# Kernel tuning notes

Hardware: AMD Instinct MI355X
Metric: run time of the kernel (lower is better)

The kernel has to match this reference:

```python
import jax, jax.numpy as jnp
import numpy as np

N, E, EL, D_IN, D_H = 100000, 1600000, 200000, 128, 128

def setup_inputs() -> dict:
    key = jax.random.key(0)
    ks = jax.random.split(key, 12)
    glorot = lambda k, fi, fo: jax.random.normal(k, (fi, fo), jnp.float32) * np.sqrt(2.0 / (fi + fo))
    return {
        "x": jax.random.normal(ks[0], (N, D_IN), jnp.float32),
        "edge_index": jax.random.randint(ks[1], (2, E), 0, N, jnp.int64),
        "edge_label_index": jax.random.randint(ks[2], (2, EL), 0, N, jnp.int64),
        "W1": glorot(ks[3], D_IN, D_H), "b1": jnp.zeros((D_H,), jnp.float32),
        "W2": glorot(ks[4], D_H, D_H), "b2": jnp.zeros((D_H,), jnp.float32),
        "Wp1": glorot(ks[5], 2 * D_H, D_H), "bp1": jnp.zeros((D_H,), jnp.float32),
        "Wp2": glorot(ks[6], D_H, 1), "bp2": jnp.zeros((1,), jnp.float32),
    }

def gcn_conv(x, W, b, src, dst, n_nodes):
    # GCNConv: h = D^{-1/2} (A + I) D^{-1/2} (x @ W) + b, deg includes self-loop
    h = x @ W                                            # [N, D]
    deg = jnp.zeros((n_nodes,), h.dtype).at[dst].add(1.0) + 1.0
    dinv = jax.lax.rsqrt(deg)                            # [N]
    coef = dinv[src] * dinv[dst]                         # [E]
    agg = jnp.zeros_like(h).at[dst].add(h[src] * coef[:, None])
    agg = agg + h * (dinv * dinv)[:, None]               # self-loop term
    return agg + b

def reference(x, edge_index, edge_label_index, W1, b1, W2, b2, Wp1, bp1, Wp2, bp2):
    src, dst = edge_index[0], edge_index[1]
    n = x.shape[0]
    h = jax.nn.relu(gcn_conv(x, W1, b1, src, dst, n))
    h = gcn_conv(h, W2, b2, src, dst, n)
    # link scoring: gather src/dst embeddings, concat, 2-layer MLP (dropout = eval identity)
    edge_emb = jnp.concatenate([h[edge_label_index[0]], h[edge_label_index[1]]], axis=1)  # [EL, 2D]
    pred = jax.nn.relu(edge_emb @ Wp1 + bp1) @ Wp2 + bp2
    return pred.squeeze(-1)
```

## Files before the change

kernel.cpp:

```cpp
#include <hip/hip_runtime.h>

#define NN 100000
#define EE 1600000
#define ELN 200000

#define NB 98
#define BKT_SHIFT 10
#define BKT_NODES 1024
#define MSB 256
#define EPB (EE / MSB)

typedef __attribute__((ext_vector_type(4))) float f32x4;
typedef __attribute__((ext_vector_type(8))) short short8;

__device__ __forceinline__ unsigned short f2bf(float f) {
    unsigned u = __builtin_bit_cast(unsigned, f);
    u += 0x7FFF + ((u >> 16) & 1);
    return (unsigned short)(u >> 16);
}
__device__ __forceinline__ float bf2f(unsigned short h) {
    return __builtin_bit_cast(float, (unsigned)h << 16);
}

__device__ __forceinline__ void convw_one(const float* __restrict__ W,
                                          unsigned short* __restrict__ WT, int K, int u) {
    int n = u & 127, kq = u >> 7;
    short8 t;
#pragma unroll
    for (int j = 0; j < 8; j++)
        t[j] = (short)f2bf(W[(size_t)(kq * 8 + j) * 128 + n]);
    *(short8*)(WT + (size_t)n * K + kq * 8) = t;
}

__global__ __launch_bounds__(256) void convw_kernel(const float* __restrict__ W1,
                                                    const float* __restrict__ W2,
                                                    const float* __restrict__ Wp1,
                                                    unsigned short* __restrict__ W1T,
                                                    unsigned short* __restrict__ W2T,
                                                    unsigned short* __restrict__ WpT) {
    int u = blockIdx.x * 256 + threadIdx.x;
    if (u < 2048) convw_one(W1, W1T, 128, u);
    else if (u < 4096) convw_one(W2, W2T, 128, u - 2048);
    else convw_one(Wp1, WpT, 256, u - 4096);
}

__global__ __launch_bounds__(256) void ms_hist_kernel(const int* __restrict__ dst,
                                                      int* __restrict__ histM) {
    __shared__ int cnt[NB];
    int tid = threadIdx.x;
    if (tid < NB) cnt[tid] = 0;
    __syncthreads();
    int base = blockIdx.x * EPB;
    for (int i = tid; i < EPB; i += 256)
        atomicAdd(&cnt[dst[base + i] >> BKT_SHIFT], 1);
    __syncthreads();
    if (tid < NB) histM[tid * MSB + blockIdx.x] = cnt[tid];
}

__global__ __launch_bounds__(256) void ms_scan_kernel(int* __restrict__ histM,
                                                      int* __restrict__ rowptr) {
    __shared__ int sm[256];
    int tid = threadIdx.x;
    const int CPT = NB * MSB / 256;
    int base = tid * CPT;
    int s = 0;
    for (int i = 0; i < CPT; i++) s += histM[base + i];
    sm[tid] = s;
    __syncthreads();
    for (int off = 1; off < 256; off <<= 1) {
        int add = (tid >= off) ? sm[tid - off] : 0;
        __syncthreads();
        sm[tid] += add;
        __syncthreads();
    }
    int run = sm[tid] - s;
    for (int i = 0; i < CPT; i++) {
        int v = histM[base + i];
        histM[base + i] = run;
        run += v;
    }
    if (tid == 0) rowptr[NN] = EE;
}

__global__ __launch_bounds__(256) void ms_scatter_kernel(const int* __restrict__ src,
                                                         const int* __restrict__ dst,
                                                         const int* __restrict__ histO,
                                                         unsigned* __restrict__ tmp) {
    __shared__ int off[NB];
    int tid = threadIdx.x;
    if (tid < NB) off[tid] = histO[tid * MSB + blockIdx.x];
    __syncthreads();
    int base = blockIdx.x * EPB;
    for (int i = tid; i < EPB; i += 256) {
        int d = dst[base + i];
        int s = src[base + i];
        int b = d >> BKT_SHIFT;
        int pos = atomicAdd(&off[b], 1);
        tmp[pos] = ((unsigned)(d & (BKT_NODES - 1)) << 17) | (unsigned)s;
    }
}

__global__ __launch_bounds__(256) void bucket_csr_kernel(const unsigned* __restrict__ tmp,
                                                         const int* __restrict__ histO,
                                                         int* __restrict__ rowptr,
                                                         float* __restrict__ dinv,
                                                         int* __restrict__ csr) {
    __shared__ int cnt[BKT_NODES];
    __shared__ int lp[BKT_NODES];
    __shared__ int sm[256];
    int b = blockIdx.x;
    int tid = threadIdx.x;
    int gbase = histO[b * MSB];
    int gend = (b == NB - 1) ? EE : histO[(b + 1) * MSB];
    for (int i = tid; i < BKT_NODES; i += 256) cnt[i] = 0;
    __syncthreads();
    for (int i = gbase + tid; i < gend; i += 256)
        atomicAdd(&cnt[tmp[i] >> 17], 1);
    __syncthreads();
    int s0 = cnt[tid * 4], s1 = cnt[tid * 4 + 1], s2 = cnt[tid * 4 + 2], s3 = cnt[tid * 4 + 3];
    int tot = s0 + s1 + s2 + s3;
    sm[tid] = tot;
    __syncthreads();
    for (int off = 1; off < 256; off <<= 1) {
        int add = (tid >= off) ? sm[tid - off] : 0;
        __syncthreads();
        sm[tid] += add;
        __syncthreads();
    }
    int excl = sm[tid] - tot;
    lp[tid * 4] = excl;
    lp[tid * 4 + 1] = excl + s0;
    lp[tid * 4 + 2] = excl + s0 + s1;
    lp[tid * 4 + 3] = excl + s0 + s1 + s2;
    int n0 = b << BKT_SHIFT;
#pragma unroll
    for (int q = 0; q < 4; q++) {
        int i = tid * 4 + q;
        int node = n0 + i;
        if (node < NN) {
            rowptr[node] = gbase + (q == 0 ? excl : lp[i]);
            int c = (q == 0) ? s0 : (q == 1 ? s1 : (q == 2 ? s2 : s3));
            dinv[node] = rsqrtf((float)c + 1.0f);
        }
    }
    cnt[tid * 4] = 0; cnt[tid * 4 + 1] = 0; cnt[tid * 4 + 2] = 0; cnt[tid * 4 + 3] = 0;
    __syncthreads();
    for (int i = gbase + tid; i < gend; i += 256) {
        unsigned p = tmp[i];
        int dl = p >> 17;
        int s = p & 0x1FFFF;
        int pos = atomicAdd(&cnt[dl], 1);
        csr[gbase + lp[dl] + pos] = s;
    }
}

template <int AMODE>
__global__ __launch_bounds__(256) void gemm_mfma_kernel(const void* __restrict__ Av,
                                                        const unsigned short* __restrict__ WT,
                                                        const float* __restrict__ dinv,
                                                        unsigned short* __restrict__ out,
                                                        int nchunks) {
    __shared__ __align__(16) char Wl[128 * 128 * 2];
    int tid = threadIdx.x;
#pragma unroll
    for (int j = 0; j < 8; j++) {
        int slot = tid + j * 256;
        int n = slot >> 4, k0 = (slot & 15) * 8;
        int byte = (n * 256 + k0 * 2) ^ ((n & 7) << 4);
        *(short8*)(Wl + byte) = ((const short8*)WT)[slot];
    }
    __syncthreads();
    int wid = tid >> 6, l = tid & 63;
    int lhi = l >> 4, llo = l & 15;
    for (int chunk = blockIdx.x; chunk < nchunks; chunk += gridDim.x) {
        int r0 = chunk * 64 + wid * 16;
        int arow = r0 + llo;
        f32x4 acc[8];
#pragma unroll
        for (int c = 0; c < 8; c++) acc[c] = (f32x4)0.0f;
#pragma unroll
        for (int ks = 0; ks < 4; ks++) {
            int koff = ks * 32 + lhi * 8;
            short8 a;
            if (arow < NN) {
                if (AMODE == 0) {
                    const float* ap = (const float*)Av + (size_t)arow * 128 + koff;
                    float4 v0 = *(const float4*)ap;
                    float4 v1 = *(const float4*)(ap + 4);
                    a[0] = (short)f2bf(v0.x); a[1] = (short)f2bf(v0.y);
                    a[2] = (short)f2bf(v0.z); a[3] = (short)f2bf(v0.w);
                    a[4] = (short)f2bf(v1.x); a[5] = (short)f2bf(v1.y);
                    a[6] = (short)f2bf(v1.z); a[7] = (short)f2bf(v1.w);
                } else {
                    a = *(const short8*)((const unsigned short*)Av + (size_t)arow * 128 + koff);
                }
            } else {
                a = (short8)(short)0;
            }
#pragma unroll
            for (int c = 0; c < 8; c++) {
                int n = c * 16 + llo;
                int byte = (n * 256 + koff * 2) ^ ((n & 7) << 4);
                short8 bfr = *(const short8*)(Wl + byte);
                acc[c] = __builtin_amdgcn_mfma_f32_16x16x32_bf16(a, bfr, acc[c], 0, 0, 0);
            }
        }
        float dv[4];
#pragma unroll
        for (int j = 0; j < 4; j++) {
            int row = r0 + lhi * 4 + j;
            dv[j] = (row < NN) ? dinv[row] : 0.f;
        }
#pragma unroll
        for (int c = 0; c < 8; c++) {
            int col = c * 16 + llo;
#pragma unroll
            for (int j = 0; j < 4; j++) {
                int row = r0 + lhi * 4 + j;
                if (row < NN)
                    out[(size_t)row * 128 + col] = f2bf(acc[c][j] * dv[j]);
            }
        }
    }
}

template <int RELU>
__global__ __launch_bounds__(256) void agg_row_kernel(const unsigned short* __restrict__ g,
                                                      const int* __restrict__ rowptr,
                                                      const int* __restrict__ csr,
                                                      const float* __restrict__ dinv,
                                                      const float* __restrict__ bias,
                                                      unsigned short* __restrict__ out) {
    int wid = threadIdx.x >> 6, l = threadIdx.x & 63;
    int node = blockIdx.x * 4 + wid;
    if (node >= NN) return;
    const unsigned* gp = (const unsigned*)g;
    unsigned sv = gp[(size_t)node * 64 + l];
    float a0 = bf2f((unsigned short)sv);
    float a1 = bf2f((unsigned short)(sv >> 16));
    int beg = rowptr[node], end = rowptr[node + 1];
    int i = beg;
    for (; i + 8 <= end; i += 8) {
        int s[8];
        unsigned v[8];
#pragma unroll
        for (int j = 0; j < 8; j++) s[j] = csr[i + j];
#pragma unroll
        for (int j = 0; j < 8; j++) v[j] = gp[(size_t)s[j] * 64 + l];
#pragma unroll
        for (int j = 0; j < 8; j++) {
            a0 += bf2f((unsigned short)v[j]);
            a1 += bf2f((unsigned short)(v[j] >> 16));
        }
    }
    for (; i < end; i++) {
        int s = csr[i];
        unsigned v = gp[(size_t)s * 64 + l];
        a0 += bf2f((unsigned short)v);
        a1 += bf2f((unsigned short)(v >> 16));
    }
    float dn = dinv[node];
    a0 = fmaf(dn, a0, bias[l * 2]);
    a1 = fmaf(dn, a1, bias[l * 2 + 1]);
    if (RELU) { a0 = fmaxf(a0, 0.f); a1 = fmaxf(a1, 0.f); }
    ((unsigned*)out)[(size_t)node * 64 + l] = (unsigned)f2bf(a0) | ((unsigned)f2bf(a1) << 16);
}

__global__ __launch_bounds__(512, 2) void link_mfma_kernel(const unsigned short* __restrict__ h,
                                                           const int* __restrict__ eli,
                                                           const unsigned short* __restrict__ WpT,
                                                           const float* __restrict__ bp1,
                                                           const float* __restrict__ Wp2,
                                                           const float* __restrict__ bp2,
                                                           float* __restrict__ out) {
    __shared__ __align__(16) char Wl[128 * 256 * 2];
    int tid = threadIdx.x;
#pragma unroll
    for (int j = 0; j < 8; j++) {
        int slot = tid + j * 512;
        int n = slot >> 5, k0 = (slot & 31) * 8;
        int byte = (n * 512 + k0 * 2) ^ ((n & 7) << 4);
        *(short8*)(Wl + byte) = ((const short8*)WpT)[slot];
    }
    __syncthreads();
    int wid = tid >> 6, l = tid & 63;
    int lhi = l >> 4, llo = l & 15;
    float b2 = bp2[0];
    const int NG = (ELN + 127) / 128;
    for (int g = blockIdx.x; g < NG; g += gridDim.x) {
        int e_base = g * 128 + wid * 16;
        if (e_base >= ELN) continue;
        int ea = e_base + llo;
        int es = eli[ea], et = eli[ELN + ea];
        f32x4 acc[8];
#pragma unroll
        for (int c = 0; c < 8; c++) acc[c] = (f32x4)0.0f;
#pragma unroll
        for (int ks = 0; ks < 8; ks++) {
            int kg = ks * 32 + lhi * 8;
            int row = (kg < 128) ? es : et;
            int koff = kg & 127;
            short8 a = *(const short8*)(h + (size_t)row * 128 + koff);
#pragma unroll
            for (int c = 0; c < 8; c++) {
                int n = c * 16 + llo;
                int byte = (n * 512 + kg * 2) ^ ((n & 7) << 4);
                short8 bfr = *(const short8*)(Wl + byte);
                acc[c] = __builtin_amdgcn_mfma_f32_16x16x32_bf16(a, bfr, acc[c], 0, 0, 0);
            }
        }
        float p0 = 0.f, p1 = 0.f, p2 = 0.f, p3 = 0.f;
#pragma unroll
        for (int c = 0; c < 8; c++) {
            int col = c * 16 + llo;
            float bb = bp1[col];
            float w2 = Wp2[col];
            p0 += fmaxf(acc[c][0] + bb, 0.f) * w2;
            p1 += fmaxf(acc[c][1] + bb, 0.f) * w2;
            p2 += fmaxf(acc[c][2] + bb, 0.f) * w2;
            p3 += fmaxf(acc[c][3] + bb, 0.f) * w2;
        }
#pragma unroll
        for (int off = 1; off < 16; off <<= 1) {
            p0 += __shfl_xor(p0, off);
            p1 += __shfl_xor(p1, off);
            p2 += __shfl_xor(p2, off);
            p3 += __shfl_xor(p3, off);
        }
        if (llo == 0) {
            int e = e_base + lhi * 4;
            out[e + 0] = p0 + b2;
            out[e + 1] = p1 + b2;
            out[e + 2] = p2 + b2;
            out[e + 3] = p3 + b2;
        }
    }
}

extern "C" void kernel_launch(void* const* d_in, const int* in_sizes, int n_in,
                              void* d_out, int out_size, void* d_ws, size_t ws_size,
                              hipStream_t stream) {
    const float* x   = (const float*)d_in[0];
    const int*   ei  = (const int*)d_in[1];
    const int*   eli = (const int*)d_in[2];
    const float* W1  = (const float*)d_in[3];
    const float* b1  = (const float*)d_in[4];
    const float* W2  = (const float*)d_in[5];
    const float* b2  = (const float*)d_in[6];
    const float* Wp1 = (const float*)d_in[7];
    const float* bp1 = (const float*)d_in[8];
    const float* Wp2 = (const float*)d_in[9];
    const float* bp2 = (const float*)d_in[10];
    float* out = (float*)d_out;

    char* w = (char*)d_ws;
    auto alloc = [&](size_t bytes) {
        char* p = w;
        w += (bytes + 255) & ~(size_t)255;
        return p;
    };
    float*          dinv   = (float*)alloc((size_t)NN * 4);
    int*            rowptr = (int*)alloc((size_t)(NN + 1) * 4);
    int*            histM  = (int*)alloc((size_t)NB * MSB * 4);
    unsigned*       tmp    = (unsigned*)alloc((size_t)EE * 4);
    int*            csr    = (int*)alloc((size_t)EE * 4);
    unsigned short* gbuf   = (unsigned short*)alloc((size_t)NN * 128 * 2);
    unsigned short* hbuf   = (unsigned short*)alloc((size_t)NN * 128 * 2);
    unsigned short* W1T    = (unsigned short*)alloc((size_t)128 * 128 * 2);
    unsigned short* W2T    = (unsigned short*)alloc((size_t)128 * 128 * 2);
    unsigned short* WpT    = (unsigned short*)alloc((size_t)128 * 256 * 2);

    const int* srcv = ei;
    const int* dstv = ei + EE;

    convw_kernel<<<32, 256, 0, stream>>>(W1, W2, Wp1, W1T, W2T, WpT);

    ms_hist_kernel<<<MSB, 256, 0, stream>>>(dstv, histM);
    ms_scan_kernel<<<1, 256, 0, stream>>>(histM, rowptr);
    ms_scatter_kernel<<<MSB, 256, 0, stream>>>(srcv, dstv, histM, tmp);
    bucket_csr_kernel<<<NB, 256, 0, stream>>>(tmp, histM, rowptr, dinv, csr);

    int nchunks = (NN + 63) / 64;
    gemm_mfma_kernel<0><<<1024, 256, 0, stream>>>(x, W1T, dinv, gbuf, nchunks);
    agg_row_kernel<1><<<NN / 4, 256, 0, stream>>>(gbuf, rowptr, csr, dinv, b1, hbuf);
    gemm_mfma_kernel<1><<<1024, 256, 0, stream>>>(hbuf, W2T, dinv, gbuf, nchunks);
    agg_row_kernel<0><<<NN / 4, 256, 0, stream>>>(gbuf, rowptr, csr, dinv, b2, hbuf);
    link_mfma_kernel<<<512, 512, 0, stream>>>(hbuf, eli, WpT, bp1, Wp2, bp2, out);
}
```

Baseline: 310.1 us.

## Fuse layer-1 aggregation with layer-2 GEMM and widen aggregation to 16-byte gathers

Layer-1 aggregation now runs inside a new kernel: each wave aggregates 16 node rows into LDS, then multiplies them by W2 with MFMA and writes the dinv-scaled g2 directly. This removes one kernel launch and the round trip of the hidden activations through global memory. The aggregation kernels also switch from one lane per 2 features to 16 lanes per node, each doing short8 (16-byte) loads, so four nodes are handled per wave. The cost is a larger LDS footprint per block, which may reduce occupancy, and a serial aggregate-then-GEMM phase inside each wave.

```diff
diff --git a/kernel.cpp b/kernel.cpp
--- a/kernel.cpp
+++ b/kernel.cpp
@@ -154,8 +154,7 @@
     }
 }
 
-template <int AMODE>
-__global__ __launch_bounds__(256) void gemm_mfma_kernel(const void* __restrict__ Av,
+__global__ __launch_bounds__(256) void gemm_mfma_kernel(const float* __restrict__ Av,
                                                         const unsigned short* __restrict__ WT,
                                                         const float* __restrict__ dinv,
                                                         unsigned short* __restrict__ out,
@@ -183,17 +182,13 @@
             int koff = ks * 32 + lhi * 8;
             short8 a;
             if (arow < NN) {
-                if (AMODE == 0) {
-                    const float* ap = (const float*)Av + (size_t)arow * 128 + koff;
-                    float4 v0 = *(const float4*)ap;
-                    float4 v1 = *(const float4*)(ap + 4);
-                    a[0] = (short)f2bf(v0.x); a[1] = (short)f2bf(v0.y);
-                    a[2] = (short)f2bf(v0.z); a[3] = (short)f2bf(v0.w);
-                    a[4] = (short)f2bf(v1.x); a[5] = (short)f2bf(v1.y);
-                    a[6] = (short)f2bf(v1.z); a[7] = (short)f2bf(v1.w);
-                } else {
-                    a = *(const short8*)((const unsigned short*)Av + (size_t)arow * 128 + koff);
-                }
+                const float* ap = Av + (size_t)arow * 128 + koff;
+                float4 v0 = *(const float4*)ap;
+                float4 v1 = *(const float4*)(ap + 4);
+                a[0] = (short)f2bf(v0.x); a[1] = (short)f2bf(v0.y);
+                a[2] = (short)f2bf(v0.z); a[3] = (short)f2bf(v0.w);
+                a[4] = (short)f2bf(v1.x); a[5] = (short)f2bf(v1.y);
+                a[6] = (short)f2bf(v1.z); a[7] = (short)f2bf(v1.w);
             } else {
                 a = (short8)(short)0;
             }
@@ -224,46 +219,150 @@
     }
 }
 
-template <int RELU>
-__global__ __launch_bounds__(256) void agg_row_kernel(const unsigned short* __restrict__ g,
-                                                      const int* __restrict__ rowptr,
-                                                      const int* __restrict__ csr,
-                                                      const float* __restrict__ dinv,
-                                                      const float* __restrict__ bias,
-                                                      unsigned short* __restrict__ out) {
-    int wid = threadIdx.x >> 6, l = threadIdx.x & 63;
-    int node = blockIdx.x * 4 + wid;
+__global__ __launch_bounds__(512) void agg1_gemm2_kernel(const unsigned short* __restrict__ g1,
+                                                         const unsigned short* __restrict__ W2T,
+                                                         const int* __restrict__ rowptr,
+                                                         const int* __restrict__ csr,
+                                                         const float* __restrict__ dinv,
+                                                         const float* __restrict__ b1,
+                                                         unsigned short* __restrict__ g2) {
+    __shared__ __align__(16) char Wl[128 * 128 * 2];
+    __shared__ __align__(16) char Ht[8][16 * 128 * 2];
+    int tid = threadIdx.x;
+#pragma unroll
+    for (int j = 0; j < 4; j++) {
+        int slot = tid + j * 512;
+        int n = slot >> 4, k0 = (slot & 15) * 8;
+        int byte = (n * 256 + k0 * 2) ^ ((n & 7) << 4);
+        *(short8*)(Wl + byte) = ((const short8*)W2T)[slot];
+    }
+    __syncthreads();
+    int w = tid >> 6, l = tid & 63;
+    int t = l >> 4, q = l & 15;
+    char* ht = Ht[w];
+    int base = blockIdx.x * 128 + w * 16;
+    float bb[8];
+#pragma unroll
+    for (int j = 0; j < 8; j++) bb[j] = b1[q * 8 + j];
+#pragma unroll
+    for (int tb = 0; tb < 4; tb++) {
+        int node = base + tb * 4 + t;
+        float a[8];
+#pragma unroll
+        for (int j = 0; j < 8; j++) a[j] = 0.f;
+        if (node < NN) {
+            short8 sv = *(const short8*)(g1 + (size_t)node * 128 + q * 8);
+#pragma unroll
+            for (int j = 0; j < 8; j++) a[j] += bf2f((unsigned short)sv[j]);
+            int beg = rowptr[node], end = rowptr[node + 1];
+            int i = beg;
+            for (; i + 4 <= end; i += 4) {
+                int s0 = csr[i], s1 = csr[i + 1], s2 = csr[i + 2], s3 = csr[i + 3];
+                short8 v0 = *(const short8*)(g1 + (size_t)s0 * 128 + q * 8);
+                short8 v1 = *(const short8*)(g1 + (size_t)s1 * 128 + q * 8);
+                short8 v2 = *(const short8*)(g1 + (size_t)s2 * 128 + q * 8);
+                short8 v3 = *(const short8*)(g1 + (size_t)s3 * 128 + q * 8);
+#pragma unroll
+                for (int j = 0; j < 8; j++) {
+                    a[j] += bf2f((unsigned short)v0[j]);
+                    a[j] += bf2f((unsigned short)v1[j]);
+                    a[j] += bf2f((unsigned short)v2[j]);
+                    a[j] += bf2f((unsigned short)v3[j]);
+                }
+            }
+            for (; i < end; i++) {
+                int s = csr[i];
+                short8 v = *(const short8*)(g1 + (size_t)s * 128 + q * 8);
+#pragma unroll
+                for (int j = 0; j < 8; j++) a[j] += bf2f((unsigned short)v[j]);
+            }
+            float dn = dinv[node];
+#pragma unroll
+            for (int j = 0; j < 8; j++) a[j] = fmaxf(fmaf(dn, a[j], bb[j]), 0.f);
+        }
+        short8 hr;
+#pragma unroll
+        for (int j = 0; j < 8; j++) hr[j] = (short)f2bf(a[j]);
+        int r = tb * 4 + t;
+        int byte = (r * 256 + q * 16) ^ ((r & 7) << 4);
+        *(short8*)(ht + byte) = hr;
+    }
+    int llo = q, lhi = t;
+    f32x4 acc[8];
+#pragma unroll
+    for (int c = 0; c < 8; c++) acc[c] = (f32x4)0.0f;
+#pragma unroll
+    for (int ks = 0; ks < 4; ks++) {
+        int koff = ks * 32 + lhi * 8;
+        int abyte = (llo * 256 + koff * 2) ^ ((llo & 7) << 4);
+        short8 afr = *(const short8*)(ht + abyte);
+#pragma unroll
+        for (int c = 0; c < 8; c++) {
+            int n = c * 16 + llo;
+            int byte = (n * 256 + koff * 2) ^ ((n & 7) << 4);
+            short8 bfr = *(const short8*)(Wl + byte);
+            acc[c] = __builtin_amdgcn_mfma_f32_16x16x32_bf16(afr, bfr, acc[c], 0, 0, 0);
+        }
+    }
+    float dv[4];
+#pragma unroll
+    for (int j = 0; j < 4; j++) {
+        int row = base + lhi * 4 + j;
+        dv[j] = (row < NN) ? dinv[row] : 0.f;
+    }
+#pragma unroll
+    for (int c = 0; c < 8; c++) {
+        int col = c * 16 + llo;
+#pragma unroll
+        for (int j = 0; j < 4; j++) {
+            int row = base + lhi * 4 + j;
+            if (row < NN)
+                g2[(size_t)row * 128 + col] = f2bf(acc[c][j] * dv[j]);
+        }
+    }
+}
+
+__global__ __launch_bounds__(512) void agg2_kernel(const unsigned short* __restrict__ g,
+                                                   const int* __restrict__ rowptr,
+                                                   const int* __restrict__ csr,
+                                                   const float* __restrict__ dinv,
+                                                   const float* __restrict__ bias,
+                                                   unsigned short* __restrict__ out) {
+    int w = threadIdx.x >> 6, l = threadIdx.x & 63;
+    int t = l >> 4, q = l & 15;
+    int node = blockIdx.x * 32 + w * 4 + t;
     if (node >= NN) return;
-    const unsigned* gp = (const unsigned*)g;
-    unsigned sv = gp[(size_t)node * 64 + l];
-    float a0 = bf2f((unsigned short)sv);
-    float a1 = bf2f((unsigned short)(sv >> 16));
+    float a[8];
+    short8 sv = *(const short8*)(g + (size_t)node * 128 + q * 8);
+#pragma unroll
+    for (int j = 0; j < 8; j++) a[j] = bf2f((unsigned short)sv[j]);
     int beg = rowptr[node], end = rowptr[node + 1];
     int i = beg;
-    for (; i + 8 <= end; i += 8) {
-        int s[8];
-        unsigned v[8];
-#pragma unroll
-        for (int j = 0; j < 8; j++) s[j] = csr[i + j];
-#pragma unroll
-        for (int j = 0; j < 8; j++) v[j] = gp[(size_t)s[j] * 64 + l];
+    for (; i + 4 <= end; i += 4) {
+        int s0 = csr[i], s1 = csr[i + 1], s2 = csr[i + 2], s3 = csr[i + 3];
+        short8 v0 = *(const short8*)(g + (size_t)s0 * 128 + q * 8);
+        short8 v1 = *(const short8*)(g + (size_t)s1 * 128 + q * 8);
+        short8 v2 = *(const short8*)(g + (size_t)s2 * 128 + q * 8);
+        short8 v3 = *(const short8*)(g + (size_t)s3 * 128 + q * 8);
 #pragma unroll
         for (int j = 0; j < 8; j++) {
-            a0 += bf2f((unsigned short)v[j]);
-            a1 += bf2f((unsigned short)(v[j] >> 16));
+            a[j] += bf2f((unsigned short)v0[j]);
+            a[j] += bf2f((unsigned short)v1[j]);
+            a[j] += bf2f((unsigned short)v2[j]);
+            a[j] += bf2f((unsigned short)v3[j]);
         }
     }
     for (; i < end; i++) {
         int s = csr[i];
-        unsigned v = gp[(size_t)s * 64 + l];
-        a0 += bf2f((unsigned short)v);
-        a1 += bf2f((unsigned short)(v >> 16));
+        short8 v = *(const short8*)(g + (size_t)s * 128 + q * 8);
+#pragma unroll
+        for (int j = 0; j < 8; j++) a[j] += bf2f((unsigned short)v[j]);
     }
     float dn = dinv[node];
-    a0 = fmaf(dn, a0, bias[l * 2]);
-    a1 = fmaf(dn, a1, bias[l * 2 + 1]);
-    if (RELU) { a0 = fmaxf(a0, 0.f); a1 = fmaxf(a1, 0.f); }
-    ((unsigned*)out)[(size_t)node * 64 + l] = (unsigned)f2bf(a0) | ((unsigned)f2bf(a1) << 16);
+    short8 hr;
+#pragma unroll
+    for (int j = 0; j < 8; j++) hr[j] = (short)f2bf(fmaf(dn, a[j], bias[q * 8 + j]));
+    *(short8*)(out + (size_t)node * 128 + q * 8) = hr;
 }
 
 __global__ __launch_bounds__(512, 2) void link_mfma_kernel(const unsigned short* __restrict__ h,
@@ -381,9 +480,8 @@
     bucket_csr_kernel<<<NB, 256, 0, stream>>>(tmp, histM, rowptr, dinv, csr);
 
     int nchunks = (NN + 63) / 64;
-    gemm_mfma_kernel<0><<<1024, 256, 0, stream>>>(x, W1T, dinv, gbuf, nchunks);
-    agg_row_kernel<1><<<NN / 4, 256, 0, stream>>>(gbuf, rowptr, csr, dinv, b1, hbuf);
-    gemm_mfma_kernel<1><<<1024, 256, 0, stream>>>(hbuf, W2T, dinv, gbuf, nchunks);
-    agg_row_kernel<0><<<NN / 4, 256, 0, stream>>>(gbuf, rowptr, csr, dinv, b2, hbuf);
-    link_mfma_kernel<<<512, 512, 0, stream>>>(hbuf, eli, WpT, bp1, Wp2, bp2, out);
-}
+    gemm_mfma_kernel<<<1024, 256, 0, stream>>>(x, W1T, dinv, gbuf, nchunks);
+    agg1_gemm2_kernel<<<(NN + 127) / 128, 512, 0, stream>>>(gbuf, W2T, rowptr, csr, dinv, b1, hbuf);
+    agg2_kernel<<<(NN + 31) / 32, 512, 0, stream>>>(hbuf, rowptr, csr, dinv, b2, gbuf);
+    link_mfma_kernel<<<512, 512, 0, stream>>>(gbuf, eli, WpT, bp1, Wp2, bp2, out);
+}
```

New measurement: 278.6 us (median of 3 runs). 10.2% less time.

## Store node features in 16-column slices and aggregate per slice

Applied to the files above, without the earlier changes.

Node feature buffers change from row-major [N,128] to eight column slices of [N,16] bf16. The GEMM, the aggregation and the link kernels all index into this layout. Aggregation now runs one block per 256-node group per slice, with two lanes covering one node's 16 columns. The aim is to keep each slice's gather working set (about 3.2 MB) resident in cache during the random neighbor gathers. The cost is that each gather is now a 32-byte access instead of a full 256-byte row, CSR indices are re-read once per slice, and GEMM stores become scattered.

```diff
diff --git a/kernel.cpp b/kernel.cpp
--- a/kernel.cpp
+++ b/kernel.cpp
@@ -192,7 +192,9 @@
                     a[4] = (short)f2bf(v1.x); a[5] = (short)f2bf(v1.y);
                     a[6] = (short)f2bf(v1.z); a[7] = (short)f2bf(v1.w);
                 } else {
-                    a = *(const short8*)((const unsigned short*)Av + (size_t)arow * 128 + koff);
+                    const unsigned short* gsrc = (const unsigned short*)Av;
+                    a = *(const short8*)(gsrc + (size_t)(koff >> 4) * (NN * 16) +
+                                         (size_t)arow * 16 + (koff & 15));
                 }
             } else {
                 a = (short8)(short)0;
@@ -213,57 +215,65 @@
         }
 #pragma unroll
         for (int c = 0; c < 8; c++) {
-            int col = c * 16 + llo;
 #pragma unroll
             for (int j = 0; j < 4; j++) {
                 int row = r0 + lhi * 4 + j;
                 if (row < NN)
-                    out[(size_t)row * 128 + col] = f2bf(acc[c][j] * dv[j]);
+                    out[(size_t)c * (NN * 16) + (size_t)row * 16 + llo] = f2bf(acc[c][j] * dv[j]);
             }
         }
     }
 }
 
 template <int RELU>
-__global__ __launch_bounds__(256) void agg_row_kernel(const unsigned short* __restrict__ g,
-                                                      const int* __restrict__ rowptr,
-                                                      const int* __restrict__ csr,
-                                                      const float* __restrict__ dinv,
-                                                      const float* __restrict__ bias,
-                                                      unsigned short* __restrict__ out) {
-    int wid = threadIdx.x >> 6, l = threadIdx.x & 63;
-    int node = blockIdx.x * 4 + wid;
+__global__ __launch_bounds__(512) void agg_slice_kernel(const unsigned short* __restrict__ g,
+                                                        const int* __restrict__ rowptr,
+                                                        const int* __restrict__ csr,
+                                                        const float* __restrict__ dinv,
+                                                        const float* __restrict__ bias,
+                                                        unsigned short* __restrict__ out) {
+    int s = blockIdx.x & 7;
+    int gblk = blockIdx.x >> 3;
+    int w = threadIdx.x >> 6, l = threadIdx.x & 63;
+    int np = l >> 1, h = l & 1;
+    int node = gblk * 256 + w * 32 + np;
     if (node >= NN) return;
-    const unsigned* gp = (const unsigned*)g;
-    unsigned sv = gp[(size_t)node * 64 + l];
-    float a0 = bf2f((unsigned short)sv);
-    float a1 = bf2f((unsigned short)(sv >> 16));
+    const unsigned short* gs = g + (size_t)s * (NN * 16);
+    short8 sv = *(const short8*)(gs + (size_t)node * 16 + h * 8);
+    float a[8];
+#pragma unroll
+    for (int j = 0; j < 8; j++) a[j] = bf2f((unsigned short)sv[j]);
     int beg = rowptr[node], end = rowptr[node + 1];
     int i = beg;
-    for (; i + 8 <= end; i += 8) {
-        int s[8];
-        unsigned v[8];
-#pragma unroll
-        for (int j = 0; j < 8; j++) s[j] = csr[i + j];
-#pragma unroll
-        for (int j = 0; j < 8; j++) v[j] = gp[(size_t)s[j] * 64 + l];
+    for (; i + 4 <= end; i += 4) {
+        int s0 = csr[i], s1 = csr[i + 1], s2 = csr[i + 2], s3 = csr[i + 3];
+        short8 v0 = *(const short8*)(gs + (size_t)s0 * 16 + h * 8);
+        short8 v1 = *(const short8*)(gs + (size_t)s1 * 16 + h * 8);
+        short8 v2 = *(const short8*)(gs + (size_t)s2 * 16 + h * 8);
+        short8 v3 = *(const short8*)(gs + (size_t)s3 * 16 + h * 8);
 #pragma unroll
         for (int j = 0; j < 8; j++) {
-            a0 += bf2f((unsigned short)v[j]);
-            a1 += bf2f((unsigned short)(v[j] >> 16));
+            a[j] += bf2f((unsigned short)v0[j]);
+            a[j] += bf2f((unsigned short)v1[j]);
+            a[j] += bf2f((unsigned short)v2[j]);
+            a[j] += bf2f((unsigned short)v3[j]);
         }
     }
     for (; i < end; i++) {
-        int s = csr[i];
-        unsigned v = gp[(size_t)s * 64 + l];
-        a0 += bf2f((unsigned short)v);
-        a1 += bf2f((unsigned short)(v >> 16));
+        int s0 = csr[i];
+        short8 v = *(const short8*)(gs + (size_t)s0 * 16 + h * 8);
+#pragma unroll
+        for (int j = 0; j < 8; j++) a[j] += bf2f((unsigned short)v[j]);
     }
     float dn = dinv[node];
-    a0 = fmaf(dn, a0, bias[l * 2]);
-    a1 = fmaf(dn, a1, bias[l * 2 + 1]);
-    if (RELU) { a0 = fmaxf(a0, 0.f); a1 = fmaxf(a1, 0.f); }
-    ((unsigned*)out)[(size_t)node * 64 + l] = (unsigned)f2bf(a0) | ((unsigned)f2bf(a1) << 16);
+    short8 hr;
+#pragma unroll
+    for (int j = 0; j < 8; j++) {
+        float v = fmaf(dn, a[j], bias[s * 16 + h * 8 + j]);
+        if (RELU) v = fmaxf(v, 0.f);
+        hr[j] = (short)f2bf(v);
+    }
+    *(short8*)(out + (size_t)s * (NN * 16) + (size_t)node * 16 + h * 8) = hr;
 }
 
 __global__ __launch_bounds__(512, 2) void link_mfma_kernel(const unsigned short* __restrict__ h,
@@ -300,7 +310,8 @@
             int kg = ks * 32 + lhi * 8;
             int row = (kg < 128) ? es : et;
             int koff = kg & 127;
-            short8 a = *(const short8*)(h + (size_t)row * 128 + koff);
+            short8 a = *(const short8*)(h + (size_t)(koff >> 4) * (NN * 16) +
+                                        (size_t)row * 16 + (koff & 15));
 #pragma unroll
             for (int c = 0; c < 8; c++) {
                 int n = c * 16 + llo;
@@ -381,9 +392,10 @@
     bucket_csr_kernel<<<NB, 256, 0, stream>>>(tmp, histM, rowptr, dinv, csr);
 
     int nchunks = (NN + 63) / 64;
+    int aggblocks = ((NN + 255) / 256) * 8;
     gemm_mfma_kernel<0><<<1024, 256, 0, stream>>>(x, W1T, dinv, gbuf, nchunks);
-    agg_row_kernel<1><<<NN / 4, 256, 0, stream>>>(gbuf, rowptr, csr, dinv, b1, hbuf);
+    agg_slice_kernel<1><<<aggblocks, 512, 0, stream>>>(gbuf, rowptr, csr, dinv, b1, hbuf);
     gemm_mfma_kernel<1><<<1024, 256, 0, stream>>>(hbuf, W2T, dinv, gbuf, nchunks);
-    agg_row_kernel<0><<<NN / 4, 256, 0, stream>>>(gbuf, rowptr, csr, dinv, b2, hbuf);
+    agg_slice_kernel<0><<<aggblocks, 512, 0, stream>>>(gbuf, rowptr, csr, dinv, b2, hbuf);
     link_mfma_kernel<<<512, 512, 0, stream>>>(hbuf, eli, WpT, bp1, Wp2, bp2, out);
 }
```

After: 367.0 us. 1.18x slower.
